# Performance work log

Measured on AMD Instinct MI355X. Metric: run time of the kernel, lower is better.

The kernel has to match this reference:

```python
import jax, jax.numpy as jnp
import numpy as np

EPS = 1e-6


def setup_inputs() -> dict:
    key = jax.random.key(0)
    k = jax.random.split(key, 6)
    B, C_in, C_out, H, W, E = 32, 256, 256, 64, 64, 1024
    x = jax.random.normal(k[0], (B, C_in, H, W), dtype=jnp.float32)
    emb = jax.random.normal(k[1], (B, E), dtype=jnp.float32)
    # adaLN Linear(E -> 2*C_in). (Module zero-inits these; random here for coverage.)
    ada_w = jax.random.normal(k[2], (2 * C_in, E), dtype=jnp.float32) * 0.02
    ada_b = jax.random.normal(k[3], (2 * C_in,), dtype=jnp.float32) * 0.02
    # 1x1 Conv2d(C_in -> C_out) weight (C_out, C_in) and bias
    conv_w = jax.random.normal(k[4], (C_out, C_in), dtype=jnp.float32) * (1.0 / np.sqrt(C_in))
    conv_b = jax.random.normal(k[5], (C_out,), dtype=jnp.float32) * 0.02
    return {"x": x, "emb": emb, "ada_w": ada_w, "ada_b": ada_b,
            "conv_w": conv_w, "conv_b": conv_b}


def reference(x, emb, ada_w, ada_b, conv_w, conv_b):
    # adaLN modulation: SiLU(emb) @ W^T + b -> (B, 2C) -> shift, scale
    mod = jax.nn.silu(emb) @ ada_w.T + ada_b          # (B, 2C)
    shift, scale = jnp.split(mod, 2, axis=1)          # each (B, C)
    # RMSNorm over channel dim (no affine)
    rms = jax.lax.rsqrt(jnp.mean(x * x, axis=1, keepdims=True) + EPS)  # (B,1,H,W)
    xn = x * rms
    # modulate: x * (1 + scale) + shift, broadcast over H,W
    xm = xn * (1.0 + scale[:, :, None, None]) + shift[:, :, None, None]
    # 1x1 conv == channel GEMM
    y = jnp.einsum('bchw,oc->bohw', xm, conv_w) + conv_b[None, :, None, None]
    return jax.nn.selu(y)
```

## Files before the change

### kernel.cpp

```cpp
#include <hip/hip_runtime.h>
#include <hip/hip_bf16.h>

typedef __attribute__((ext_vector_type(4))) float f32x4;
typedef __attribute__((ext_vector_type(8))) short s16x8;
typedef __attribute__((ext_vector_type(4))) unsigned short u16x4;

__device__ __forceinline__ unsigned short f2bf(float f) {
  unsigned u = __builtin_bit_cast(unsigned, f);
  u += 0x7fffu + ((u >> 16) & 1u);
  return (unsigned short)(u >> 16);
}

__global__ __launch_bounds__(512) void k_mod(const float* __restrict__ emb,
                                             const float* __restrict__ ada_w,
                                             const float* __restrict__ ada_b,
                                             float* __restrict__ mod) {
  __shared__ __align__(16) float semb[32][1028];
  const int t = threadIdx.x;
  for (int i = t; i < 8192; i += 512) {
    f32x4 v = ((const f32x4*)emb)[i];
    f32x4 s;
#pragma unroll
    for (int j = 0; j < 4; ++j) s[j] = v[j] / (1.f + __expf(-v[j]));
    *(f32x4*)&semb[i >> 8][(i & 255) << 2] = s;
  }
  __syncthreads();
  const int jl = t >> 5, b = t & 31;
  const int j = blockIdx.x * 16 + jl;
  const f32x4* aw = (const f32x4*)(ada_w + (size_t)j * 1024);
  float acc = 0.f;
  for (int q = 0; q < 256; ++q) {
    f32x4 a = aw[q];
    f32x4 sv = *(const f32x4*)&semb[b][q * 4];
    acc += a[0] * sv[0] + a[1] * sv[1] + a[2] * sv[2] + a[3] * sv[3];
  }
  mod[b * 512 + j] = acc + ada_b[j];
}

__global__ __launch_bounds__(256) void k_prep(const float* __restrict__ mod,
                                              const float* __restrict__ conv_w,
                                              const float* __restrict__ conv_b,
                                              unsigned short* __restrict__ wp,
                                              float* __restrict__ dvec) {
  const int b = blockIdx.y;
  const int o = blockIdx.x * 4 + (threadIdx.x >> 6);
  const int l = threadIdx.x & 63;
  const float* sh = mod + b * 512;
  const float* sc = mod + b * 512 + 256;
  f32x4 cw = ((const f32x4*)(conv_w + (size_t)o * 256))[l];
  f32x4 s4 = ((const f32x4*)sc)[l];
  f32x4 h4 = ((const f32x4*)sh)[l];
  u16x4 wq;
#pragma unroll
  for (int j = 0; j < 4; ++j) wq[j] = f2bf(cw[j] * (1.f + s4[j]));
  const int wr = o >> 6, m = (o >> 4) & 3, lr = o & 15;
  const int kk = l >> 3, g = (l >> 1) & 3, jb = 4 * (l & 1);
  *(u16x4*)(wp + (size_t)b * 65536 + (((wr * 4 + m) * 8 + kk) * 512 + g * 128 + lr * 8 + jb)) = wq;
  float dd = cw[0] * h4[0] + cw[1] * h4[1] + cw[2] * h4[2] + cw[3] * h4[3];
#pragma unroll
  for (int off = 32; off; off >>= 1) dd += __shfl_down(dd, off);
  if (l == 0) dvec[b * 256 + o] = dd + conv_b[o];
}

__global__ __launch_bounds__(512, 4) void k_main(const float* __restrict__ x,
                                                 const unsigned short* __restrict__ wp,
                                                 const float* __restrict__ dvec,
                                                 float* __restrict__ out) {
  constexpr int HW = 4096;
  __shared__ __align__(16) unsigned short lds_bt[64 * 256];
  __shared__ float lds_part[8][64];
  __shared__ float lds_rms[64];
  __shared__ float lds_d[256];

  const int t = threadIdx.x;
  const int b = blockIdx.y;
  const int s0 = blockIdx.x * 64;
  const int w = t >> 6, lane = t & 63;
  const int wr = w >> 1, wc = w & 1;
  const int lr = lane & 15, g = lane >> 4;

  const unsigned short* A2 = wp + (size_t)b * 65536;

  if (t < 256) lds_d[t] = dvec[b * 256 + t];

  const float* xb = x + (size_t)b * (256 * HW) + s0;
  const int sq = t & 15, cg = t >> 4;
  f32x4 sacc = {0.f, 0.f, 0.f, 0.f};
#pragma unroll
  for (int it = 0; it < 8; ++it) {
    int c = cg + 32 * it;
    f32x4 v = *(const f32x4*)(xb + (size_t)c * HW + 4 * sq);
    sacc += v * v;
#pragma unroll
    for (int r = 0; r < 4; ++r) {
      int s = 4 * sq + r;
      lds_bt[s * 256 + (c ^ (((s >> 1) & 7) << 3))] = f2bf(v[r]);
    }
  }
#pragma unroll
  for (int off = 16; off <= 32; off <<= 1) {
#pragma unroll
    for (int j = 0; j < 4; ++j) sacc[j] += __shfl_xor(sacc[j], off);
  }
  if (lane < 16) *(f32x4*)&lds_part[w][4 * sq] = sacc;
  __syncthreads();
  if (t < 64) {
    float sum = 0.f;
#pragma unroll
    for (int q = 0; q < 8; ++q) sum += lds_part[q][t];
    lds_rms[t] = rsqrtf(sum * (1.0f / 256.0f) + 1e-6f);
  }
  __syncthreads();

  f32x4 acc[4][2] = {};
  const int sA = 32 * wc + lr;
  const int sB = sA + 16;

#pragma unroll
  for (int kk = 0; kk < 8; ++kk) {
    s16x8 af[4];
#pragma unroll
    for (int m = 0; m < 4; ++m)
      af[m] = *(const s16x8*)(A2 + (((wr * 4 + m) * 8 + kk) * 512 + lane * 8));

    const int c0 = kk * 32 + g * 8;
    s16x8 b0 = *(const s16x8*)&lds_bt[sA * 256 + (c0 ^ (((sA >> 1) & 7) << 3))];
    s16x8 b1 = *(const s16x8*)&lds_bt[sB * 256 + (c0 ^ (((sB >> 1) & 7) << 3))];

#pragma unroll
    for (int m = 0; m < 4; ++m) {
      acc[m][0] = __builtin_amdgcn_mfma_f32_16x16x32_bf16(af[m], b0, acc[m][0], 0, 0, 0);
      acc[m][1] = __builtin_amdgcn_mfma_f32_16x16x32_bf16(af[m], b1, acc[m][1], 0, 0, 0);
    }
  }

  float* ob = out + (size_t)b * (256 * HW) + s0;
#pragma unroll
  for (int m = 0; m < 4; ++m) {
    const int o0 = 64 * wr + 16 * m + 4 * g;
#pragma unroll
    for (int n = 0; n < 2; ++n) {
      const int s = 32 * wc + 16 * n + lr;
      const float rr = lds_rms[s];
#pragma unroll
      for (int r = 0; r < 4; ++r) {
        float v = rr * acc[m][n][r] + lds_d[o0 + r];
        float res = v > 0.f ? 1.0507009873554805f * v
                            : 1.7580993408473766f * expm1f(v);
        ob[(size_t)(o0 + r) * HW + s] = res;
      }
    }
  }
}

extern "C" void kernel_launch(void* const* d_in, const int* in_sizes, int n_in,
                              void* d_out, int out_size, void* d_ws, size_t ws_size,
                              hipStream_t stream) {
  const float* x      = (const float*)d_in[0];
  const float* emb    = (const float*)d_in[1];
  const float* ada_w  = (const float*)d_in[2];
  const float* ada_b  = (const float*)d_in[3];
  const float* conv_w = (const float*)d_in[4];
  const float* conv_b = (const float*)d_in[5];
  float* out = (float*)d_out;

  float* mod  = (float*)d_ws;
  float* dvec = mod + 32 * 512;
  unsigned short* wp = (unsigned short*)(dvec + 32 * 256);

  k_mod<<<dim3(32), 512, 0, stream>>>(emb, ada_w, ada_b, mod);
  k_prep<<<dim3(64, 32), 256, 0, stream>>>(mod, conv_w, conv_b, wp, dvec);
  k_main<<<dim3(64, 32), 512, 0, stream>>>(x, wp, dvec, out);
}
```

Measured before the change: 101.0 us.

## Software-pipeline MFMA fragment loads, move barrier after GEMM, use fast exp in SELU

Double-buffers the A fragments (global) and B fragments (LDS) so the loads for the next k-step are issued while the current step's MFMAs run. The second barrier moves from before the GEMM to after it, so the GEMM overlaps the RMS reduction. The launch-bounds occupancy hint drops from 4 to 2, giving the compiler more registers for the extra buffers. The epilogue reads dvec as one vector and replaces expm1f with __expf(v)-1, which costs some accuracy near zero.

```diff
diff --git a/kernel.cpp b/kernel.cpp
--- a/kernel.cpp
+++ b/kernel.cpp
@@ -62,7 +62,7 @@
   if (l == 0) dvec[b * 256 + o] = dd + conv_b[o];
 }
 
-__global__ __launch_bounds__(512, 4) void k_main(const float* __restrict__ x,
+__global__ __launch_bounds__(512, 2) void k_main(const float* __restrict__ x,
                                                  const unsigned short* __restrict__ wp,
                                                  const float* __restrict__ dvec,
                                                  float* __restrict__ out) {
@@ -110,43 +110,60 @@
     for (int q = 0; q < 8; ++q) sum += lds_part[q][t];
     lds_rms[t] = rsqrtf(sum * (1.0f / 256.0f) + 1e-6f);
   }
-  __syncthreads();
 
   f32x4 acc[4][2] = {};
   const int sA = 32 * wc + lr;
   const int sB = sA + 16;
+  const unsigned swA = ((sA >> 1) & 7) << 3;
+  const unsigned swB = ((sB >> 1) & 7) << 3;
+
+  s16x8 afc[4], afn[4], b0c, b1c, b0n, b1n;
+#pragma unroll
+  for (int m = 0; m < 4; ++m)
+    afc[m] = *(const s16x8*)(A2 + (((wr * 4 + m) * 8 + 0) * 512 + lane * 8));
+  {
+    const int c0 = 0 * 32 + g * 8;
+    b0c = *(const s16x8*)&lds_bt[sA * 256 + (c0 ^ swA)];
+    b1c = *(const s16x8*)&lds_bt[sB * 256 + (c0 ^ swB)];
+  }
 
 #pragma unroll
   for (int kk = 0; kk < 8; ++kk) {
-    s16x8 af[4];
+    if (kk < 7) {
 #pragma unroll
-    for (int m = 0; m < 4; ++m)
-      af[m] = *(const s16x8*)(A2 + (((wr * 4 + m) * 8 + kk) * 512 + lane * 8));
-
-    const int c0 = kk * 32 + g * 8;
-    s16x8 b0 = *(const s16x8*)&lds_bt[sA * 256 + (c0 ^ (((sA >> 1) & 7) << 3))];
-    s16x8 b1 = *(const s16x8*)&lds_bt[sB * 256 + (c0 ^ (((sB >> 1) & 7) << 3))];
-
+      for (int m = 0; m < 4; ++m)
+        afn[m] = *(const s16x8*)(A2 + (((wr * 4 + m) * 8 + kk + 1) * 512 + lane * 8));
+      const int c1 = (kk + 1) * 32 + g * 8;
+      b0n = *(const s16x8*)&lds_bt[sA * 256 + (c1 ^ swA)];
+      b1n = *(const s16x8*)&lds_bt[sB * 256 + (c1 ^ swB)];
+    }
 #pragma unroll
     for (int m = 0; m < 4; ++m) {
-      acc[m][0] = __builtin_amdgcn_mfma_f32_16x16x32_bf16(af[m], b0, acc[m][0], 0, 0, 0);
-      acc[m][1] = __builtin_amdgcn_mfma_f32_16x16x32_bf16(af[m], b1, acc[m][1], 0, 0, 0);
+      acc[m][0] = __builtin_amdgcn_mfma_f32_16x16x32_bf16(afc[m], b0c, acc[m][0], 0, 0, 0);
+      acc[m][1] = __builtin_amdgcn_mfma_f32_16x16x32_bf16(afc[m], b1c, acc[m][1], 0, 0, 0);
     }
+#pragma unroll
+    for (int m = 0; m < 4; ++m) afc[m] = afn[m];
+    b0c = b0n;
+    b1c = b1n;
   }
+
+  __syncthreads();
 
   float* ob = out + (size_t)b * (256 * HW) + s0;
 #pragma unroll
   for (int m = 0; m < 4; ++m) {
     const int o0 = 64 * wr + 16 * m + 4 * g;
+    const f32x4 dv = *(const f32x4*)&lds_d[o0];
 #pragma unroll
     for (int n = 0; n < 2; ++n) {
       const int s = 32 * wc + 16 * n + lr;
       const float rr = lds_rms[s];
 #pragma unroll
       for (int r = 0; r < 4; ++r) {
-        float v = rr * acc[m][n][r] + lds_d[o0 + r];
+        float v = rr * acc[m][n][r] + dv[r];
         float res = v > 0.f ? 1.0507009873554805f * v
-                            : 1.7580993408473766f * expm1f(v);
+                            : 1.7580993408473766f * (__expf(v) - 1.f);
         ob[(size_t)(o0 + r) * HW + s] = res;
       }
     }
```

Result: faster. 96.82 us (-4.2%).

## Split fused main kernel into transpose/RMS prepass and larger-tile GEMM kernel

Applied to the files above, without the earlier changes.

The fused kernel, which loaded x, transposed it to bf16 in LDS, computed RMS and ran the GEMM, is split in two. The first kernel writes a transposed bf16 copy of x and per-pixel rms values to the workspace. The second kernel reads B fragments straight from global memory, uses a 64x64 tile per wave, and swaps expm1f for __expf-1. This adds a full round trip of the bf16 x (about 64MB written and read) and an extra launch, in exchange for better MFMA reuse. The prepass also writes 2-byte values scattered with a 512-byte stride, which is uncoalesced.

```diff
diff --git a/kernel.cpp b/kernel.cpp
--- a/kernel.cpp
+++ b/kernel.cpp
@@ -62,92 +62,104 @@
   if (l == 0) dvec[b * 256 + o] = dd + conv_b[o];
 }
 
-__global__ __launch_bounds__(512, 4) void k_main(const float* __restrict__ x,
-                                                 const unsigned short* __restrict__ wp,
-                                                 const float* __restrict__ dvec,
-                                                 float* __restrict__ out) {
+__global__ __launch_bounds__(512) void k_pre(const float* __restrict__ x,
+                                             unsigned short* __restrict__ xT,
+                                             float* __restrict__ rms_g) {
   constexpr int HW = 4096;
-  __shared__ __align__(16) unsigned short lds_bt[64 * 256];
-  __shared__ float lds_part[8][64];
-  __shared__ float lds_rms[64];
-  __shared__ float lds_d[256];
-
+  __shared__ float part[8][256];
   const int t = threadIdx.x;
   const int b = blockIdx.y;
-  const int s0 = blockIdx.x * 64;
+  const int s0 = blockIdx.x * 256;
   const int w = t >> 6, lane = t & 63;
-  const int wr = w >> 1, wc = w & 1;
-  const int lr = lane & 15, g = lane >> 4;
+  const int cl = t >> 4;
+  const int sq = t & 15;
+  const float* xb = x + (size_t)b * (256 * HW) + s0;
+  unsigned short* xTb = xT + ((size_t)b * HW + s0) * 256;
 
-  const unsigned short* A2 = wp + (size_t)b * 65536;
-
-  if (t < 256) lds_d[t] = dvec[b * 256 + t];
-
-  const float* xb = x + (size_t)b * (256 * HW) + s0;
-  const int sq = t & 15, cg = t >> 4;
-  f32x4 sacc = {0.f, 0.f, 0.f, 0.f};
+  f32x4 ss[4] = {};
 #pragma unroll
-  for (int it = 0; it < 8; ++it) {
-    int c = cg + 32 * it;
-    f32x4 v = *(const f32x4*)(xb + (size_t)c * HW + 4 * sq);
-    sacc += v * v;
+  for (int cc = 0; cc < 8; ++cc) {
+    const int c = cc * 32 + cl;
+    const float* row = xb + (size_t)c * HW;
 #pragma unroll
-    for (int r = 0; r < 4; ++r) {
-      int s = 4 * sq + r;
-      lds_bt[s * 256 + (c ^ (((s >> 1) & 7) << 3))] = f2bf(v[r]);
+    for (int si = 0; si < 4; ++si) {
+      f32x4 v = *(const f32x4*)(row + si * 64 + 4 * sq);
+      ss[si] += v * v;
+#pragma unroll
+      for (int r = 0; r < 4; ++r)
+        xTb[(size_t)(si * 64 + 4 * sq + r) * 256 + c] = f2bf(v[r]);
     }
   }
 #pragma unroll
   for (int off = 16; off <= 32; off <<= 1) {
 #pragma unroll
-    for (int j = 0; j < 4; ++j) sacc[j] += __shfl_xor(sacc[j], off);
+    for (int si = 0; si < 4; ++si)
+#pragma unroll
+      for (int j = 0; j < 4; ++j) ss[si][j] += __shfl_xor(ss[si][j], off);
   }
-  if (lane < 16) *(f32x4*)&lds_part[w][4 * sq] = sacc;
+  if (lane < 16) {
+#pragma unroll
+    for (int si = 0; si < 4; ++si) *(f32x4*)&part[w][si * 64 + 4 * sq] = ss[si];
+  }
   __syncthreads();
-  if (t < 64) {
+  if (t < 256) {
     float sum = 0.f;
 #pragma unroll
-    for (int q = 0; q < 8; ++q) sum += lds_part[q][t];
-    lds_rms[t] = rsqrtf(sum * (1.0f / 256.0f) + 1e-6f);
+    for (int q = 0; q < 8; ++q) sum += part[q][t];
+    rms_g[(size_t)b * HW + s0 + t] = rsqrtf(sum * (1.0f / 256.0f) + 1e-6f);
   }
-  __syncthreads();
+}
 
-  f32x4 acc[4][2] = {};
-  const int sA = 32 * wc + lr;
-  const int sB = sA + 16;
+__global__ __launch_bounds__(512, 4) void k_gemm(const unsigned short* __restrict__ xT,
+                                                 const unsigned short* __restrict__ wp,
+                                                 const float* __restrict__ rms_g,
+                                                 const float* __restrict__ dvec,
+                                                 float* __restrict__ out) {
+  constexpr int HW = 4096;
+  const int t = threadIdx.x;
+  const int b = blockIdx.y;
+  const int w = t >> 6, lane = t & 63;
+  const int wr = w >> 1, wc = w & 1;
+  const int lr = lane & 15, g = lane >> 4;
+  const int s0 = blockIdx.x * 128 + wc * 64;
 
+  const unsigned short* A2 = wp + (size_t)b * 65536;
+  const unsigned short* Bb = xT + ((size_t)b * HW + s0) * 256;
+
+  f32x4 acc[4][4] = {};
 #pragma unroll
   for (int kk = 0; kk < 8; ++kk) {
     s16x8 af[4];
 #pragma unroll
     for (int m = 0; m < 4; ++m)
       af[m] = *(const s16x8*)(A2 + (((wr * 4 + m) * 8 + kk) * 512 + lane * 8));
-
-    const int c0 = kk * 32 + g * 8;
-    s16x8 b0 = *(const s16x8*)&lds_bt[sA * 256 + (c0 ^ (((sA >> 1) & 7) << 3))];
-    s16x8 b1 = *(const s16x8*)&lds_bt[sB * 256 + (c0 ^ (((sB >> 1) & 7) << 3))];
-
+    s16x8 bf[4];
 #pragma unroll
-    for (int m = 0; m < 4; ++m) {
-      acc[m][0] = __builtin_amdgcn_mfma_f32_16x16x32_bf16(af[m], b0, acc[m][0], 0, 0, 0);
-      acc[m][1] = __builtin_amdgcn_mfma_f32_16x16x32_bf16(af[m], b1, acc[m][1], 0, 0, 0);
-    }
+    for (int n = 0; n < 4; ++n)
+      bf[n] = *(const s16x8*)(Bb + (size_t)(16 * n + lr) * 256 + kk * 32 + g * 8);
+#pragma unroll
+    for (int m = 0; m < 4; ++m)
+#pragma unroll
+      for (int n = 0; n < 4; ++n)
+        acc[m][n] = __builtin_amdgcn_mfma_f32_16x16x32_bf16(af[m], bf[n], acc[m][n], 0, 0, 0);
   }
 
+  float rr[4];
+#pragma unroll
+  for (int n = 0; n < 4; ++n) rr[n] = rms_g[(size_t)b * HW + s0 + 16 * n + lr];
   float* ob = out + (size_t)b * (256 * HW) + s0;
 #pragma unroll
   for (int m = 0; m < 4; ++m) {
     const int o0 = 64 * wr + 16 * m + 4 * g;
+    const f32x4 dv = *(const f32x4*)(dvec + (size_t)b * 256 + o0);
 #pragma unroll
-    for (int n = 0; n < 2; ++n) {
-      const int s = 32 * wc + 16 * n + lr;
-      const float rr = lds_rms[s];
+    for (int n = 0; n < 4; ++n) {
 #pragma unroll
       for (int r = 0; r < 4; ++r) {
-        float v = rr * acc[m][n][r] + lds_d[o0 + r];
+        float v = rr[n] * acc[m][n][r] + dv[r];
         float res = v > 0.f ? 1.0507009873554805f * v
-                            : 1.7580993408473766f * expm1f(v);
-        ob[(size_t)(o0 + r) * HW + s] = res;
+                            : 1.7580993408473766f * (__expf(v) - 1.f);
+        ob[(size_t)(o0 + r) * HW + 16 * n + lr] = res;
       }
     }
   }
@@ -164,11 +176,14 @@
   const float* conv_b = (const float*)d_in[5];
   float* out = (float*)d_out;
 
-  float* mod  = (float*)d_ws;
-  float* dvec = mod + 32 * 512;
-  unsigned short* wp = (unsigned short*)(dvec + 32 * 256);
+  float* mod   = (float*)d_ws;
+  float* dvec  = mod + 32 * 512;
+  float* rms_g = dvec + 32 * 256;
+  unsigned short* wp = (unsigned short*)(rms_g + 32 * 4096);
+  unsigned short* xT = wp + (size_t)32 * 256 * 256;
 
   k_mod<<<dim3(32), 512, 0, stream>>>(emb, ada_w, ada_b, mod);
   k_prep<<<dim3(64, 32), 256, 0, stream>>>(mod, conv_w, conv_b, wp, dvec);
-  k_main<<<dim3(64, 32), 512, 0, stream>>>(x, wp, dvec, out);
+  k_pre<<<dim3(16, 32), 512, 0, stream>>>(x, xT, rms_g);
+  k_gemm<<<dim3(32, 32), 512, 0, stream>>>(xT, wp, rms_g, dvec, out);
 }
```

Measured after the change: 215.4 us. 2.13x slower.

## Stage x loads via async global_load_lds double buffer and defer rms sync

Applied to the files above, without the earlier changes.

Loads of x now go through a per-wave double-buffered LDS staging area using async global-to-LDS loads with explicit vmcnt waits, then a transpose into the bf16 B tile that also accumulates the sum of squares. The second barrier is moved after the MFMA loop so the GEMM overlaps with the rms computation. The bias now comes straight from global memory instead of a shared copy, and expm1f is replaced by __expf minus one. The aim is more memory-level parallelism and less barrier stall, at the cost of about 8 KB of extra LDS, which may reduce occupancy, and slightly less accurate SELU on the negative side.

```diff
diff --git a/kernel.cpp b/kernel.cpp
--- a/kernel.cpp
+++ b/kernel.cpp
@@ -67,42 +67,80 @@
                                                  const float* __restrict__ dvec,
                                                  float* __restrict__ out) {
   constexpr int HW = 4096;
+  __shared__ __align__(16) unsigned char stg[8 * 2 * 2 * 1056];
   __shared__ __align__(16) unsigned short lds_bt[64 * 256];
   __shared__ float lds_part[8][64];
   __shared__ float lds_rms[64];
-  __shared__ float lds_d[256];
 
   const int t = threadIdx.x;
   const int b = blockIdx.y;
   const int s0 = blockIdx.x * 64;
   const int w = t >> 6, lane = t & 63;
-  const int wr = w >> 1, wc = w & 1;
-  const int lr = lane & 15, g = lane >> 4;
-
-  const unsigned short* A2 = wp + (size_t)b * 65536;
-
-  if (t < 256) lds_d[t] = dvec[b * 256 + t];
 
   const float* xb = x + (size_t)b * (256 * HW) + s0;
-  const int sq = t & 15, cg = t >> 4;
-  f32x4 sacc = {0.f, 0.f, 0.f, 0.f};
-#pragma unroll
-  for (int it = 0; it < 8; ++it) {
-    int c = cg + 32 * it;
-    f32x4 v = *(const f32x4*)(xb + (size_t)c * HW + 4 * sq);
-    sacc += v * v;
-#pragma unroll
-    for (int r = 0; r < 4; ++r) {
-      int s = 4 * sq + r;
-      lds_bt[s * 256 + (c ^ (((s >> 1) & 7) << 3))] = f2bf(v[r]);
-    }
-  }
-#pragma unroll
-  for (int off = 16; off <= 32; off <<= 1) {
-#pragma unroll
-    for (int j = 0; j < 4; ++j) sacc[j] += __shfl_xor(sacc[j], off);
-  }
-  if (lane < 16) *(f32x4*)&lds_part[w][4 * sq] = sacc;
+  unsigned char* stg_w = stg + w * (2 * 2112);
+
+  float ss[8] = {0.f, 0.f, 0.f, 0.f, 0.f, 0.f, 0.f, 0.f};
+
+#define ISSUE(Q, SLOT)                                                                   \
+  {                                                                                      \
+    _Pragma("unroll") for (int i = 0; i < 2; ++i) {                                      \
+      const float* gp = xb + (size_t)((Q)*64 + w * 8 + i * 4 + (lane >> 4)) * HW +       \
+                        (lane & 15) * 4;                                                 \
+      void* lp = stg_w + (SLOT)*2112 + i * 1056;                                         \
+      __builtin_amdgcn_global_load_lds((const __attribute__((address_space(1))) void*)gp,\
+                                       (__attribute__((address_space(3))) void*)lp, 16,  \
+                                       0, 0);                                            \
+    }                                                                                    \
+  }
+
+#define TRANS(Q, SLOT)                                                                   \
+  {                                                                                      \
+    const int r = lane >> 3;                                                             \
+    const float* sp =                                                                    \
+        (const float*)(stg_w + (SLOT)*2112 + (r >> 2) * 1056 + (r & 3) * 256 +           \
+                       (lane & 7) * 32);                                                 \
+    f32x4 v0 = *(const f32x4*)sp;                                                        \
+    f32x4 v1 = *((const f32x4*)sp + 1);                                                  \
+    const int c = (Q)*64 + w * 8 + r;                                                    \
+    const int sb = (lane & 7) * 8;                                                       \
+    _Pragma("unroll") for (int j = 0; j < 4; ++j) {                                      \
+      int s = sb + j;                                                                    \
+      lds_bt[s * 256 + (c ^ (((s >> 1) & 7) << 3))] = f2bf(v0[j]);                       \
+      ss[j] += v0[j] * v0[j];                                                            \
+    }                                                                                    \
+    _Pragma("unroll") for (int j = 0; j < 4; ++j) {                                      \
+      int s = sb + 4 + j;                                                                \
+      lds_bt[s * 256 + (c ^ (((s >> 1) & 7) << 3))] = f2bf(v1[j]);                       \
+      ss[4 + j] += v1[j] * v1[j];                                                        \
+    }                                                                                    \
+  }
+
+  ISSUE(0, 0);
+  ISSUE(1, 1);
+  asm volatile("s_waitcnt vmcnt(2)" ::: "memory");
+  TRANS(0, 0);
+  ISSUE(2, 0);
+  asm volatile("s_waitcnt vmcnt(2)" ::: "memory");
+  TRANS(1, 1);
+  ISSUE(3, 1);
+  asm volatile("s_waitcnt vmcnt(2)" ::: "memory");
+  TRANS(2, 0);
+  asm volatile("s_waitcnt vmcnt(0)" ::: "memory");
+  TRANS(3, 1);
+#undef ISSUE
+#undef TRANS
+
+#pragma unroll
+  for (int off = 8; off <= 32; off <<= 1) {
+#pragma unroll
+    for (int j = 0; j < 8; ++j) ss[j] += __shfl_xor(ss[j], off);
+  }
+  if (lane < 8) {
+    f32x4 p0 = {ss[0], ss[1], ss[2], ss[3]}, p1 = {ss[4], ss[5], ss[6], ss[7]};
+    *(f32x4*)&lds_part[w][lane * 8] = p0;
+    *(f32x4*)&lds_part[w][lane * 8 + 4] = p1;
+  }
   __syncthreads();
   if (t < 64) {
     float sum = 0.f;
@@ -110,11 +148,15 @@
     for (int q = 0; q < 8; ++q) sum += lds_part[q][t];
     lds_rms[t] = rsqrtf(sum * (1.0f / 256.0f) + 1e-6f);
   }
-  __syncthreads();
-
+
+  const unsigned short* A2 = wp + (size_t)b * 65536;
+  const int wr = w >> 1, wc = w & 1;
+  const int lr = lane & 15, g = lane >> 4;
   f32x4 acc[4][2] = {};
   const int sA = 32 * wc + lr;
   const int sB = sA + 16;
+  const unsigned swA = ((sA >> 1) & 7) << 3;
+  const unsigned swB = ((sB >> 1) & 7) << 3;
 
 #pragma unroll
   for (int kk = 0; kk < 8; ++kk) {
@@ -124,8 +166,8 @@
       af[m] = *(const s16x8*)(A2 + (((wr * 4 + m) * 8 + kk) * 512 + lane * 8));
 
     const int c0 = kk * 32 + g * 8;
-    s16x8 b0 = *(const s16x8*)&lds_bt[sA * 256 + (c0 ^ (((sA >> 1) & 7) << 3))];
-    s16x8 b1 = *(const s16x8*)&lds_bt[sB * 256 + (c0 ^ (((sB >> 1) & 7) << 3))];
+    s16x8 b0 = *(const s16x8*)&lds_bt[sA * 256 + (c0 ^ swA)];
+    s16x8 b1 = *(const s16x8*)&lds_bt[sB * 256 + (c0 ^ swB)];
 
 #pragma unroll
     for (int m = 0; m < 4; ++m) {
@@ -134,19 +176,22 @@
     }
   }
 
+  __syncthreads();
+
   float* ob = out + (size_t)b * (256 * HW) + s0;
 #pragma unroll
   for (int m = 0; m < 4; ++m) {
     const int o0 = 64 * wr + 16 * m + 4 * g;
+    const f32x4 dv = *(const f32x4*)(dvec + (size_t)b * 256 + o0);
 #pragma unroll
     for (int n = 0; n < 2; ++n) {
       const int s = 32 * wc + 16 * n + lr;
       const float rr = lds_rms[s];
 #pragma unroll
       for (int r = 0; r < 4; ++r) {
-        float v = rr * acc[m][n][r] + lds_d[o0 + r];
+        float v = rr * acc[m][n][r] + dv[r];
         float res = v > 0.f ? 1.0507009873554805f * v
-                            : 1.7580993408473766f * expm1f(v);
+                            : 1.7580993408473766f * (__expf(v) - 1.f);
         ob[(size_t)(o0 + r) * HW + s] = res;
       }
     }
```

Result: no change. 99.26 us (-1.8%).
